# Optimization experiments

Measured on AMD Instinct MI355X. Metric: run time of the kernel, lower is better.

## Reference

```python
import jax, jax.numpy as jnp
from jax import lax
import numpy as np

B, H, W, C = 64, 64, 64, 8          # batch, grid, channel_n (C=8 is structurally required)
PC = 3 * C                           # perceive output channels = 24
FIRE_RATE = 0.5
ALPHA_THR = 0.1

def _conv(x, w, b, padding):
    y = lax.conv_general_dilated(x, w, (1, 1), padding,
                                 dimension_numbers=('NHWC', 'HWIO', 'NHWC'))
    return y + b

def _dwconv(x, k):
    # k: [kh, kw, Cin, mult] (TF depthwise layout) -> grouped conv rhs [kh, kw, 1, Cin*mult]
    kh, kw, cin, m = k.shape
    rhs = k.reshape(kh, kw, 1, cin * m)
    return lax.conv_general_dilated(x, rhs, (1, 1), 'SAME',
                                    dimension_numbers=('NHWC', 'HWIO', 'NHWC'),
                                    feature_group_count=cin)

def _maxpool3(a):
    return lax.reduce_window(a, -jnp.inf, lax.max, (1, 3, 3, 1), (1, 1, 1, 1), 'SAME')

def setup_inputs() -> dict:
    key = jax.random.key(0)
    ks = jax.random.split(key, 12)
    d_flat = H * W * PC                       # 98304
    d_att = 3 * 3 * 24 * 3                    # 648
    s = lambda *sh: 0.02
    return {
        'x': jax.random.normal(ks[0], (B, H, W, C), jnp.float32),
        'update_noise': jax.random.uniform(ks[1], (B, H, W, 1), jnp.float32),
        'W_att': jax.random.normal(ks[2], (d_flat, d_att), jnp.float32) * 0.002,
        'b_att': jax.random.normal(ks[3], (d_att,), jnp.float32) * 0.02,
        'W1': jax.random.normal(ks[4], (3, 3, 3 * PC, 48), jnp.float32) * 0.05,
        'b1': jax.random.normal(ks[5], (48,), jnp.float32) * 0.02,
        'Wt': jax.random.normal(ks[6], (3, 3, 48, 48), jnp.float32) * 0.05,
        'bt': jax.random.normal(ks[7], (48,), jnp.float32) * 0.02,
        'W2': jax.random.normal(ks[8], (1, 1, 48, 128), jnp.float32) * 0.05,
        'b2': jax.random.normal(ks[9], (128,), jnp.float32) * 0.02,
        'W3': jax.random.normal(ks[10], (1, 1, 128, C), jnp.float32) * 0.05,
        'b3': jax.random.normal(ks[11], (C,), jnp.float32) * 0.02,
    }

def reference(x, update_noise, W_att, b_att, W1, b1, Wt, bt, W2, b2, W3, b3):
    # --- fixed perceive stencil (angle = 0) ---
    ident = np.outer(np.float32([0, 1, 0]), np.float32([0, 1, 0]))
    dxk = np.outer(np.float32([1, 0, 1]), np.float32([1, 0, 1])) / 8.0
    dyk = dxk.T
    k = jnp.stack([jnp.asarray(ident), jnp.asarray(dxk), jnp.asarray(dyk)], -1)  # [3,3,3]
    k = jnp.tile(k[:, :, None, :], (1, 1, C, 1))                                 # [3,3,C,3]

    pre_life = _maxpool3(x[:, :, :, 3:4]) > ALPHA_THR

    y = _dwconv(x, k)                                     # [B,H,W,24]
    # global attention: flatten -> dense -> reshape, take sample 0's kernel
    y_sum = (y.reshape(y.shape[0], -1) @ W_att + b_att).reshape(-1, 3, 3, 24, 3)[0]
    y = _dwconv(y, y_sum)                                 # [B,H,W,72]
    y = y * lax.rsqrt(jnp.maximum(jnp.sum(y * y), 1e-12))  # global l2_normalize

    # dmodel: conv3 VALID -> convT3 VALID -> 1x1 relu -> 1x1
    h = _conv(y, W1, b1, 'VALID')                         # [B,62,62,48]
    h = lax.conv_transpose(h, Wt, (1, 1), 'VALID',
                           dimension_numbers=('NHWC', 'HWIO', 'NHWC')) + bt  # [B,64,64,48]
    h = jax.nn.relu(_conv(h, W2, b2, 'SAME'))             # [B,64,64,128]
    dx_out = _conv(h, W3, b3, 'SAME')                     # [B,64,64,C], step_size = 1.0

    update_mask = (update_noise <= FIRE_RATE).astype(x.dtype)
    x2 = x + dx_out * update_mask

    post_life = _maxpool3(x2[:, :, :, 3:4]) > ALPHA_THR
    life = jnp.logical_and(pre_life, post_life).astype(x.dtype)
    return x2 * life
```

## Files before the change

kernel.cpp:

```cpp
#include <hip/hip_runtime.h>

#define NB 64
#define HW 4096

__global__ __launch_bounds__(256) void k_perceive(
    const float* __restrict__ x, float* __restrict__ y_chw,
    float* __restrict__ y0_hwc, float* __restrict__ prelife,
    float* __restrict__ att_zero, const float* __restrict__ W2,
    float* __restrict__ W2T) {
  int t = threadIdx.x;
  if (blockIdx.x == 1024) {
    for (int i = t; i < 6144; i += 256) {
      int o = i / 48;
      int c = i - o * 48;
      W2T[i] = W2[c * 128 + o];
    }
    return;
  }
  if (blockIdx.x == 0) {
    for (int i = t; i < 649; i += 256) att_zero[i] = 0.f;
  }
  int pix = blockIdx.x * 256 + t;
  int b = pix >> 12;
  int hw = pix & 4095;
  int h = hw >> 6, w = hw & 63;
  const float* xp = x + (size_t)pix * 8;
  bool hm = h > 0, hp = h < 63, wm = w > 0, wp = w < 63;

  float mx = -1e30f;
  #pragma unroll
  for (int di = -1; di <= 1; ++di) {
    if ((unsigned)(h + di) > 63u) continue;
    #pragma unroll
    for (int dj = -1; dj <= 1; ++dj) {
      if ((unsigned)(w + dj) > 63u) continue;
      mx = fmaxf(mx, xp[(di * 64 + dj) * 8 + 3]);
    }
  }
  prelife[pix] = (mx > 0.1f) ? 1.f : 0.f;

  float* yb = y_chw + (size_t)b * 16 * HW + hw;
  bool b0 = (b == 0);
  #pragma unroll
  for (int c = 0; c < 8; ++c) {
    float ctr = xp[c];
    float a00 = (hm && wm) ? xp[(-65) * 8 + c] : 0.f;
    float a02 = (hm && wp) ? xp[(-63) * 8 + c] : 0.f;
    float a20 = (hp && wm) ? xp[(63) * 8 + c] : 0.f;
    float a22 = (hp && wp) ? xp[(65) * 8 + c] : 0.f;
    float d = (a00 + a02 + a20 + a22) * 0.125f;
    yb[(size_t)(c * 2 + 0) * HW] = ctr;
    yb[(size_t)(c * 2 + 1) * HW] = d;
    if (b0) {
      float* y0p = y0_hwc + hw * 24 + c * 3;
      y0p[0] = ctr; y0p[1] = d; y0p[2] = d;
    }
  }
}

__global__ __launch_bounds__(256) void k_att(
    const float* __restrict__ y0, const float* __restrict__ Watt,
    float* __restrict__ att_acc) {
  int t = threadIdx.x;
  int r0 = blockIdx.x * 64;
  float a0 = 0.f, a1 = 0.f, a2 = 0.f;
  float b0 = 0.f, b1 = 0.f, b2 = 0.f;
  for (int r = 0; r < 64; r += 2) {
    float yv0 = y0[r0 + r];
    float yv1 = y0[r0 + r + 1];
    const float* w0 = Watt + (size_t)(r0 + r) * 648;
    const float* w1 = w0 + 648;
    a0 = fmaf(yv0, w0[t], a0);
    b0 = fmaf(yv1, w1[t], b0);
    a1 = fmaf(yv0, w0[t + 256], a1);
    b1 = fmaf(yv1, w1[t + 256], b1);
    if (t < 136) {
      a2 = fmaf(yv0, w0[t + 512], a2);
      b2 = fmaf(yv1, w1[t + 512], b2);
    }
  }
  atomicAdd(att_acc + t, a0 + b0);
  atomicAdd(att_acc + t + 256, a1 + b1);
  if (t < 136) atomicAdd(att_acc + t + 512, a2 + b2);
}

__global__ __launch_bounds__(256) void k_ssqfold(
    const float* __restrict__ y_chw, const float* __restrict__ att_acc,
    const float* __restrict__ b_att, float* __restrict__ ssq,
    const float* __restrict__ W1, float* __restrict__ K16) {
  __shared__ float ys[648];
  __shared__ float s[16 * 324];
  int t = threadIdx.x;

  if (blockIdx.x >= 1024) {
    for (int i = t; i < 648; i += 256) ys[i] = att_acc[i] + b_att[i];
    __syncthreads();
    int r = blockIdx.x - 1024;
    int ri = r / 5, rj = r - ri * 5;
    #pragma unroll
    for (int k = 0; k < 3; ++k) {
      int idx = t + 256 * k;
      int p = idx / 48;
      int o = idx - p * 48;
      int c = p >> 1, tt = p & 1;
      float acc = 0.f;
      for (int ki = 0; ki < 3; ++ki) {
        int qi = ri - ki;
        if ((unsigned)qi > 2u) continue;
        for (int kj = 0; kj < 3; ++kj) {
          int qj = rj - kj;
          if ((unsigned)qj > 2u) continue;
          int k9 = ki * 3 + kj, q9 = qi * 3 + qj;
          const float* wb = W1 + (size_t)(k9 * 72 + 9 * c) * 48 + o;
          const float* yb = ys + q9 * 72 + 9 * c;
          if (tt == 0) {
            #pragma unroll
            for (int m = 0; m < 3; ++m) acc = fmaf(wb[(size_t)m * 48], yb[m], acc);
          } else {
            #pragma unroll
            for (int m = 0; m < 3; ++m) {
              acc = fmaf(wb[(size_t)(3 + m) * 48], yb[3 + m], acc);
              acc = fmaf(wb[(size_t)(6 + m) * 48], yb[6 + m], acc);
            }
          }
        }
      }
      K16[(size_t)(r * 16 + p) * 48 + o] = acc;
    }
    return;
  }

  for (int i = t; i < 648; i += 256) ys[i] = att_acc[i] + b_att[i];

  int blk = blockIdx.x;
  int b = blk >> 4;
  int tile = blk & 15;
  int i0 = (tile >> 2) * 16;
  int j0 = (tile & 3) * 16;
  const float* yb = y_chw + (size_t)b * 16 * HW;

  for (int idx = t; idx < 16 * 324; idx += 256) {
    int c = idx / 324;
    int pos = idx - c * 324;
    int r = pos / 18, col = pos - r * 18;
    int gr = i0 - 1 + r, gc = j0 - 1 + col;
    bool v = ((unsigned)gr < 64u) && ((unsigned)gc < 64u);
    s[idx] = v ? yb[(size_t)c * HW + gr * 64 + gc] : 0.f;
  }
  __syncthreads();

  int ty = t >> 4, tx = t & 15;
  float local = 0.f;
  for (int c = 0; c < 8; ++c) {
    float tapA[9], tapB[9];
    const float* sa = s + (size_t)(2 * c) * 324 + ty * 18 + tx;
    const float* sb = s + (size_t)(2 * c + 1) * 324 + ty * 18 + tx;
    #pragma unroll
    for (int di = 0; di < 3; ++di)
      #pragma unroll
      for (int dj = 0; dj < 3; ++dj) {
        tapA[di * 3 + dj] = sa[di * 18 + dj];
        tapB[di * 3 + dj] = sb[di * 18 + dj];
      }
    #pragma unroll
    for (int m = 0; m < 3; ++m) {
      float z0 = 0.f, z1 = 0.f, z2 = 0.f;
      #pragma unroll
      for (int k9 = 0; k9 < 9; ++k9) {
        z0 = fmaf(tapA[k9], ys[k9 * 72 + 9 * c + m], z0);
        z1 = fmaf(tapB[k9], ys[k9 * 72 + 9 * c + 3 + m], z1);
        z2 = fmaf(tapB[k9], ys[k9 * 72 + 9 * c + 6 + m], z2);
      }
      local += z0 * z0 + z1 * z1 + z2 * z2;
    }
  }
  #pragma unroll
  for (int off = 32; off; off >>= 1) local += __shfl_down(local, off, 64);
  if ((t & 63) == 0) atomicAdd(ssq, local);
}

__global__ __launch_bounds__(256, 4) void k_conv1f(
    const float* __restrict__ y_chw, const float* __restrict__ K16,
    const float* __restrict__ b1, const float* __restrict__ ssqp,
    float* __restrict__ h1) {
  __shared__ float s[16 * 400];
  int t = threadIdx.x;
  int og = __builtin_amdgcn_readfirstlane(t >> 7);
  int sub = t & 127;
  int ty = sub >> 4, tx = sub & 15;
  int blk = blockIdx.x;
  int b = blk >> 4;
  int tile = blk & 15;
  int i0 = (tile >> 2) * 16; if (i0 > 46) i0 = 46;
  int j0 = (tile & 3) * 16;  if (j0 > 46) j0 = 46;

  const float* yb = y_chw + (size_t)b * 16 * HW;
  for (int idx = t; idx < 16 * 400; idx += 256) {
    int c = idx / 400;
    int pos = idx - c * 400;
    int r = pos / 20, col = pos - r * 20;
    int gr = i0 - 1 + r, gc = j0 - 1 + col;
    bool v = ((unsigned)gr < 64u) && ((unsigned)gc < 64u);
    s[idx] = v ? yb[(size_t)c * HW + gr * 64 + gc] : 0.f;
  }
  __syncthreads();

  float acc0[24], acc1[24];
  #pragma unroll
  for (int o = 0; o < 24; ++o) { acc0[o] = 0.f; acc1[o] = 0.f; }

  for (int c = 0; c < 16; ++c) {
    const float* sc = s + (size_t)c * 400 + ty * 20 + tx;
    #pragma unroll
    for (int ri = 0; ri < 5; ++ri) {
      float t0[5], t1[5];
      #pragma unroll
      for (int rj = 0; rj < 5; ++rj) {
        t0[rj] = sc[ri * 20 + rj];
        t1[rj] = sc[(ri + 8) * 20 + rj];
      }
      #pragma unroll
      for (int rj = 0; rj < 5; ++rj) {
        const float* w = K16 + (size_t)((ri * 5 + rj) * 16 + c) * 48 + og * 24;
        float tv0 = t0[rj], tv1 = t1[rj];
        #pragma unroll
        for (int o = 0; o < 24; ++o) {
          acc0[o] = fmaf(tv0, w[o], acc0[o]);
          acc1[o] = fmaf(tv1, w[o], acc1[o]);
        }
      }
    }
  }
  float inv = rsqrtf(fmaxf(ssqp[0], 1e-12f));
  float* hb = h1 + (size_t)b * 48 * 3844 + (size_t)og * 24 * 3844
            + (i0 + ty) * 62 + (j0 + tx);
  #pragma unroll
  for (int o = 0; o < 24; ++o) {
    float bo = b1[og * 24 + o];
    hb[(size_t)o * 3844] = fmaf(acc0[o], inv, bo);
    hb[(size_t)o * 3844 + 8 * 62] = fmaf(acc1[o], inv, bo);
  }
}

__global__ __launch_bounds__(256, 4) void k_convTh(
    const float* __restrict__ h1, const float* __restrict__ Wt,
    const float* __restrict__ bt, const float* __restrict__ W2T,
    const float* __restrict__ b2, const float* __restrict__ W3,
    const float* __restrict__ b3, const float* __restrict__ x,
    const float* __restrict__ noise, float* __restrict__ x2,
    float* __restrict__ alpha2) {
  __shared__ float s[24 * 324];
  int t = threadIdx.x;
  int og = __builtin_amdgcn_readfirstlane(t >> 7);
  int sub = t & 127;
  int ty = sub >> 4, tx = sub & 15;
  int blk = blockIdx.x;
  int b = blk >> 4;
  int tile = blk & 15;
  int i0 = (tile >> 2) * 16;
  int j0 = (tile & 3) * 16;

  float acc0[24], acc1[24];
  #pragma unroll
  for (int o = 0; o < 24; ++o) { acc0[o] = 0.f; acc1[o] = 0.f; }
  const float* hb = h1 + (size_t)b * 48 * 3844;

  for (int c0 = 0; c0 < 48; c0 += 24) {
    __syncthreads();
    for (int idx = t; idx < 24 * 324; idx += 256) {
      int c = idx / 324;
      int pos = idx - c * 324;
      int r = pos / 18, col = pos - r * 18;
      int gr = i0 - 2 + r, gc = j0 - 2 + col;
      bool v = ((unsigned)gr < 62u) && ((unsigned)gc < 62u);
      s[idx] = v ? hb[(size_t)(c0 + c) * 3844 + gr * 62 + gc] : 0.f;
    }
    __syncthreads();
    for (int c = 0; c < 24; ++c) {
      const float* sc = s + c * 324 + ty * 18 + tx;
      float tap0[9], tap1[9];
      #pragma unroll
      for (int di = 0; di < 3; ++di)
        #pragma unroll
        for (int dj = 0; dj < 3; ++dj) {
          tap0[di * 3 + dj] = sc[di * 18 + dj];
          tap1[di * 3 + dj] = sc[(di + 8) * 18 + dj];
        }
      #pragma unroll
      for (int k9 = 0; k9 < 9; ++k9) {
        const float* w = Wt + (size_t)(k9 * 48 + c0 + c) * 48 + og * 24;
        float tv0 = tap0[k9], tv1 = tap1[k9];
        #pragma unroll
        for (int o = 0; o < 24; ++o) {
          acc0[o] = fmaf(tv0, w[o], acc0[o]);
          acc1[o] = fmaf(tv1, w[o], acc1[o]);
        }
      }
    }
  }

  float hr[48];
  #pragma unroll
  for (int ph = 0; ph < 2; ++ph) {
    __syncthreads();
    if (og == ph) {
      #pragma unroll
      for (int o = 0; o < 24; ++o) {
        float bo = bt[ph * 24 + o];
        s[o * 256 + ty * 16 + tx] = acc0[o] + bo;
        s[o * 256 + (ty + 8) * 16 + tx] = acc1[o] + bo;
      }
    }
    __syncthreads();
    #pragma unroll
    for (int c = 0; c < 24; ++c) hr[ph * 24 + c] = s[c * 256 + t];
  }

  int pty = t >> 4, ptx = t & 15;
  int pix = b * 4096 + (i0 + pty) * 64 + (j0 + ptx);
  float dx[8];
  #pragma unroll
  for (int k = 0; k < 8; ++k) dx[k] = b3[k];
  #pragma unroll 4
  for (int o = 0; o < 128; ++o) {
    float v = b2[o];
    const float* w2 = W2T + o * 48;
    #pragma unroll
    for (int c = 0; c < 48; ++c) v = fmaf(hr[c], w2[c], v);
    v = fmaxf(v, 0.f);
    const float* w3 = W3 + o * 8;
    #pragma unroll
    for (int k = 0; k < 8; ++k) dx[k] = fmaf(v, w3[k], dx[k]);
  }
  float m = (noise[pix] <= 0.5f) ? 1.f : 0.f;
  const float* xp = x + (size_t)pix * 8;
  float* xo = x2 + (size_t)pix * 8;
  float a3 = 0.f;
  #pragma unroll
  for (int k = 0; k < 8; ++k) {
    float v = fmaf(dx[k], m, xp[k]);
    xo[k] = v;
    if (k == 3) a3 = v;
  }
  alpha2[pix] = a3;
}

__global__ __launch_bounds__(256) void k_life(
    const float* __restrict__ x2, const float* __restrict__ alpha2,
    const float* __restrict__ prelife, float* __restrict__ out) {
  int pix = blockIdx.x * 256 + threadIdx.x;
  int hw = pix & 4095;
  int h = hw >> 6, w = hw & 63;
  const float* ab = alpha2 + (size_t)(pix - hw);
  float mx = -1e30f;
  #pragma unroll
  for (int di = -1; di <= 1; ++di) {
    if ((unsigned)(h + di) > 63u) continue;
    #pragma unroll
    for (int dj = -1; dj <= 1; ++dj) {
      if ((unsigned)(w + dj) > 63u) continue;
      mx = fmaxf(mx, ab[(h + di) * 64 + (w + dj)]);
    }
  }
  float life = (mx > 0.1f && prelife[pix] > 0.5f) ? 1.f : 0.f;
  const float* xp = x2 + (size_t)pix * 8;
  float* op = out + (size_t)pix * 8;
  #pragma unroll
  for (int k = 0; k < 8; ++k) op[k] = xp[k] * life;
}

extern "C" void kernel_launch(void* const* d_in, const int* in_sizes, int n_in,
                              void* d_out, int out_size, void* d_ws, size_t ws_size,
                              hipStream_t stream) {
  const float* x     = (const float*)d_in[0];
  const float* noise = (const float*)d_in[1];
  const float* Watt  = (const float*)d_in[2];
  const float* b_att = (const float*)d_in[3];
  const float* W1    = (const float*)d_in[4];
  const float* b1    = (const float*)d_in[5];
  const float* Wt    = (const float*)d_in[6];
  const float* bt    = (const float*)d_in[7];
  const float* W2    = (const float*)d_in[8];
  const float* b2    = (const float*)d_in[9];
  const float* W3    = (const float*)d_in[10];
  const float* b3    = (const float*)d_in[11];
  float* out = (float*)d_out;

  float* ws = (float*)d_ws;
  size_t o_y   = 0;
  size_t o_h1  = o_y + 4194304;
  size_t o_y0  = o_h1 + 11808768;
  size_t o_pre = o_y0 + 98304;
  size_t o_att = o_pre + 262144;
  size_t o_w2t = o_att + 652;
  size_t o_k16 = o_w2t + 6144;
  float* y_chw   = ws + o_y;
  float* h1_chw  = ws + o_h1;
  float* y0_hwc  = ws + o_y0;
  float* prelife = ws + o_pre;
  float* att_acc = ws + o_att;
  float* ssq     = ws + o_att + 648;
  float* W2T     = ws + o_w2t;
  float* K16     = ws + o_k16;
  float* x2      = ws + o_y;
  float* alpha2  = ws + o_y + 2097152;

  k_perceive<<<1025, 256, 0, stream>>>(x, y_chw, y0_hwc, prelife, att_acc, W2, W2T);
  k_att<<<1536, 256, 0, stream>>>(y0_hwc, Watt, att_acc);
  k_ssqfold<<<1049, 256, 0, stream>>>(y_chw, att_acc, b_att, ssq, W1, K16);
  k_conv1f<<<1024, 256, 0, stream>>>(y_chw, K16, b1, ssq, h1_chw);
  k_convTh<<<1024, 256, 0, stream>>>(h1_chw, Wt, bt, W2T, b2, W3, b3, x, noise, x2, alpha2);
  k_life<<<1024, 256, 0, stream>>>(x2, alpha2, prelife, out);
}
```

Baseline: 831.2 us.

## Run folded 5x5 conv1 on MFMA with split-bf16 three-pass emulation

The conv1 kernel, formerly scalar FP32 FMAs over a folded 5x5x16 to 48 kernel, now runs as an implicit GEMM on 16x16x32 bf16 MFMA instructions. Both operands are split into high and low bf16 parts, and three MFMA passes (hh, hl, lh) approximate FP32 accuracy. The folded weights are emitted by k_ssqfold in transposed, padded bf16 hi/lo layout, and the input tile is staged in shared memory as channel-interleaved bf16 pairs. This trades extra conversion work and slightly reduced precision for much higher matrix throughput in what is likely the dominant FLOP kernel.

```diff
diff --git a/kernel.cpp b/kernel.cpp
--- a/kernel.cpp
+++ b/kernel.cpp
@@ -2,6 +2,14 @@
 
 #define NB 64
 #define HW 4096
+
+typedef __attribute__((ext_vector_type(8))) short short8;
+typedef __attribute__((ext_vector_type(4))) float f32x4;
+
+__device__ __forceinline__ unsigned short bf16_rn(float v) {
+  unsigned int u = __float_as_uint(v);
+  return (unsigned short)((u + 0x7fffu + ((u >> 16) & 1u)) >> 16);
+}
 
 __global__ __launch_bounds__(256) void k_perceive(
     const float* __restrict__ x, float* __restrict__ y_chw,
@@ -87,7 +95,8 @@
 __global__ __launch_bounds__(256) void k_ssqfold(
     const float* __restrict__ y_chw, const float* __restrict__ att_acc,
     const float* __restrict__ b_att, float* __restrict__ ssq,
-    const float* __restrict__ W1, float* __restrict__ K16) {
+    const float* __restrict__ W1, unsigned short* __restrict__ K16H,
+    unsigned short* __restrict__ K16L) {
   __shared__ float ys[648];
   __shared__ float s[16 * 324];
   int t = threadIdx.x;
@@ -125,7 +134,15 @@
           }
         }
       }
-      K16[(size_t)(r * 16 + p) * 48 + o] = acc;
+      unsigned short hb_ = bf16_rn(acc);
+      float fhi = __uint_as_float(((unsigned int)hb_) << 16);
+      unsigned short lb_ = bf16_rn(acc - fhi);
+      K16H[o * 416 + r * 16 + p] = hb_;
+      K16L[o * 416 + r * 16 + p] = lb_;
+      if (r == 24) {
+        K16H[o * 416 + 400 + p] = 0;
+        K16L[o * 416 + 400 + p] = 0;
+      }
     }
     return;
   }
@@ -180,14 +197,12 @@
 }
 
 __global__ __launch_bounds__(256, 4) void k_conv1f(
-    const float* __restrict__ y_chw, const float* __restrict__ K16,
-    const float* __restrict__ b1, const float* __restrict__ ssqp,
-    float* __restrict__ h1) {
-  __shared__ float s[16 * 400];
+    const float* __restrict__ y_chw, const unsigned short* __restrict__ K16H,
+    const unsigned short* __restrict__ K16L, const float* __restrict__ b1,
+    const float* __restrict__ ssqp, float* __restrict__ h1) {
+  __shared__ short sh[2 * 6656];
   int t = threadIdx.x;
-  int og = __builtin_amdgcn_readfirstlane(t >> 7);
-  int sub = t & 127;
-  int ty = sub >> 4, tx = sub & 15;
+  int w = t >> 6, lane = t & 63;
   int blk = blockIdx.x;
   int b = blk >> 4;
   int tile = blk & 15;
@@ -201,44 +216,69 @@
     int r = pos / 20, col = pos - r * 20;
     int gr = i0 - 1 + r, gc = j0 - 1 + col;
     bool v = ((unsigned)gr < 64u) && ((unsigned)gc < 64u);
-    s[idx] = v ? yb[(size_t)c * HW + gr * 64 + gc] : 0.f;
+    float val = v ? yb[(size_t)c * HW + gr * 64 + gc] : 0.f;
+    unsigned short hb_ = bf16_rn(val);
+    float fhi = __uint_as_float(((unsigned int)hb_) << 16);
+    unsigned short lb_ = bf16_rn(val - fhi);
+    sh[pos * 16 + c] = (short)hb_;
+    sh[6656 + pos * 16 + c] = (short)lb_;
+  }
+  if (t < 256) {
+    sh[6400 + t] = 0;
+    sh[6656 + 6400 + t] = 0;
   }
   __syncthreads();
 
-  float acc0[24], acc1[24];
-  #pragma unroll
-  for (int o = 0; o < 24; ++o) { acc0[o] = 0.f; acc1[o] = 0.f; }
-
-  for (int c = 0; c < 16; ++c) {
-    const float* sc = s + (size_t)c * 400 + ty * 20 + tx;
-    #pragma unroll
-    for (int ri = 0; ri < 5; ++ri) {
-      float t0[5], t1[5];
-      #pragma unroll
-      for (int rj = 0; rj < 5; ++rj) {
-        t0[rj] = sc[ri * 20 + rj];
-        t1[rj] = sc[(ri + 8) * 20 + rj];
-      }
-      #pragma unroll
-      for (int rj = 0; rj < 5; ++rj) {
-        const float* w = K16 + (size_t)((ri * 5 + rj) * 16 + c) * 48 + og * 24;
-        float tv0 = t0[rj], tv1 = t1[rj];
-        #pragma unroll
-        for (int o = 0; o < 24; ++o) {
-          acc0[o] = fmaf(tv0, w[o], acc0[o]);
-          acc1[o] = fmaf(tv1, w[o], acc1[o]);
-        }
-      }
-    }
-  }
+  f32x4 acc[4][3];
+  #pragma unroll
+  for (int m = 0; m < 4; ++m)
+    #pragma unroll
+    for (int n = 0; n < 3; ++n) acc[m][n] = (f32x4){0.f, 0.f, 0.f, 0.f};
+
+  int lanecol = lane & 15;
+  int half = (lane >> 4) >> 1;
+  int c0 = ((lane >> 4) & 1) * 8;
+
+  for (int ks = 0; ks < 13; ++ks) {
+    short8 bh[3], bl[3];
+    #pragma unroll
+    for (int n = 0; n < 3; ++n) {
+      int o = n * 16 + lanecol;
+      size_t boff = (size_t)o * 416 + ks * 32 + (lane >> 4) * 8;
+      bh[n] = *(const short8*)(K16H + boff);
+      bl[n] = *(const short8*)(K16L + boff);
+    }
+    int tap = 2 * ks + half;
+    int ri = tap / 5, rj = tap - ri * 5;
+    int aoff = (ri * 20 + rj + lanecol) * 16 + c0;
+    #pragma unroll
+    for (int m = 0; m < 4; ++m) {
+      int mt = (w << 2) + m;
+      int ao = aoff + mt * 320;
+      short8 ah = *(const short8*)(sh + ao);
+      short8 al = *(const short8*)(sh + 6656 + ao);
+      #pragma unroll
+      for (int n = 0; n < 3; ++n) {
+        acc[m][n] = __builtin_amdgcn_mfma_f32_16x16x32_bf16(ah, bh[n], acc[m][n], 0, 0, 0);
+        acc[m][n] = __builtin_amdgcn_mfma_f32_16x16x32_bf16(ah, bl[n], acc[m][n], 0, 0, 0);
+        acc[m][n] = __builtin_amdgcn_mfma_f32_16x16x32_bf16(al, bh[n], acc[m][n], 0, 0, 0);
+      }
+    }
+  }
+
   float inv = rsqrtf(fmaxf(ssqp[0], 1e-12f));
-  float* hb = h1 + (size_t)b * 48 * 3844 + (size_t)og * 24 * 3844
-            + (i0 + ty) * 62 + (j0 + tx);
-  #pragma unroll
-  for (int o = 0; o < 24; ++o) {
-    float bo = b1[og * 24 + o];
-    hb[(size_t)o * 3844] = fmaf(acc0[o], inv, bo);
-    hb[(size_t)o * 3844 + 8 * 62] = fmaf(acc1[o], inv, bo);
+  int rg = lane >> 4;
+  #pragma unroll
+  for (int n = 0; n < 3; ++n) {
+    int o = n * 16 + lanecol;
+    float bo = b1[o];
+    #pragma unroll
+    for (int m = 0; m < 4; ++m) {
+      int mt = (w << 2) + m;
+      float* hp = h1 + ((size_t)b * 48 + o) * 3844 + (i0 + mt) * 62 + j0 + rg * 4;
+      #pragma unroll
+      for (int r = 0; r < 4; ++r) hp[r] = fmaf(acc[m][n][r], inv, bo);
+    }
   }
 }
 
@@ -393,7 +433,8 @@
   size_t o_pre = o_y0 + 98304;
   size_t o_att = o_pre + 262144;
   size_t o_w2t = o_att + 652;
-  size_t o_k16 = o_w2t + 6144;
+  size_t o_kh  = o_w2t + 6144;
+  size_t o_kl  = o_kh + 9984;
   float* y_chw   = ws + o_y;
   float* h1_chw  = ws + o_h1;
   float* y0_hwc  = ws + o_y0;
@@ -401,14 +442,15 @@
   float* att_acc = ws + o_att;
   float* ssq     = ws + o_att + 648;
   float* W2T     = ws + o_w2t;
-  float* K16     = ws + o_k16;
+  unsigned short* K16H = (unsigned short*)(ws + o_kh);
+  unsigned short* K16L = (unsigned short*)(ws + o_kl);
   float* x2      = ws + o_y;
   float* alpha2  = ws + o_y + 2097152;
 
   k_perceive<<<1025, 256, 0, stream>>>(x, y_chw, y0_hwc, prelife, att_acc, W2, W2T);
   k_att<<<1536, 256, 0, stream>>>(y0_hwc, Watt, att_acc);
-  k_ssqfold<<<1049, 256, 0, stream>>>(y_chw, att_acc, b_att, ssq, W1, K16);
-  k_conv1f<<<1024, 256, 0, stream>>>(y_chw, K16, b1, ssq, h1_chw);
+  k_ssqfold<<<1049, 256, 0, stream>>>(y_chw, att_acc, b_att, ssq, W1, K16H, K16L);
+  k_conv1f<<<1024, 256, 0, stream>>>(y_chw, K16H, K16L, b1, ssq, h1_chw);
   k_convTh<<<1024, 256, 0, stream>>>(h1_chw, Wt, bt, W2T, b2, W3, b3, x, noise, x2, alpha2);
   k_life<<<1024, 256, 0, stream>>>(x2, alpha2, prelife, out);
 }
```

After: 753.2 us. 1.1x faster.
